# Optimization experiments

Measured on AMD Instinct MI355X. Metric: run time of the kernel, lower is better.

Reference implementation:

```python
import jax, jax.numpy as jnp
import numpy as np

N_NODES = 100000
N_EDGES = 1600000
IN_DIM, HID, OUT_DIM = 128, 64, 1


def _sage_conv(x, src, dst, wl, wr, b, num_nodes):
    # PyG SAGEConv (aggr='mean', root_weight=True):
    #   out = lin_l(mean_{j in N(i)} x_j) + lin_r(x_i), bias lives in lin_l
    msgs = x[src]                                                  # [E, d] gather
    agg = jax.ops.segment_sum(msgs, dst, num_segments=num_nodes)  # [N, d]
    deg = jax.ops.segment_sum(jnp.ones((src.shape[0],), x.dtype), dst,
                              num_segments=num_nodes)              # [N]
    agg = agg / jnp.maximum(deg, 1.0)[:, None]                     # mean aggregation
    return agg @ wl + x @ wr + b


def setup_inputs() -> dict:
    key = jax.random.key(0)
    ks = jax.random.split(key, 12)
    x = jax.random.normal(ks[0], (N_NODES, IN_DIM), dtype=jnp.float32)
    edge_index = jax.random.randint(ks[1], (2, N_EDGES), 0, N_NODES, dtype=jnp.int64)

    def glorot(k, fan_in, fan_out):
        s = jnp.sqrt(2.0 / (fan_in + fan_out)).astype(jnp.float32)
        return jax.random.normal(k, (fan_in, fan_out), dtype=jnp.float32) * s

    return {
        "x": x,
        "edge_index": edge_index,
        "wl0": glorot(ks[2], IN_DIM, HID), "wr0": glorot(ks[3], IN_DIM, HID),
        "b0": jnp.zeros((HID,), jnp.float32),
        "wl1": glorot(ks[4], HID, HID), "wr1": glorot(ks[5], HID, HID),
        "b1": jnp.zeros((HID,), jnp.float32),
        "wl2": glorot(ks[6], HID, OUT_DIM), "wr2": glorot(ks[7], HID, OUT_DIM),
        "b2": jnp.zeros((OUT_DIM,), jnp.float32),
    }


def reference(x, edge_index, wl0, wr0, b0, wl1, wr1, b1, wl2, wr2, b2):
    src, dst = edge_index[0], edge_index[1]
    n = x.shape[0]
    # layer 0: conv -> relu (dropout is identity in eval mode)
    h = jax.nn.relu(_sage_conv(x, src, dst, wl0, wr0, b0, n))
    # layer 1
    h = jax.nn.relu(_sage_conv(h, src, dst, wl1, wr1, b1, n))
    # final layer + sigmoid
    h = _sage_conv(h, src, dst, wl2, wr2, b2, n)
    return jax.nn.sigmoid(h)
```

## Files before the change

kernel.cpp:

```cpp
#include <hip/hip_runtime.h>
#include <hip/hip_bf16.h>
#include <math.h>


#define SHIFT 7
#define BKT 128
#define CHUNK 4096

typedef __bf16 bf16_t;
typedef bf16_t bf16x8 __attribute__((ext_vector_type(8)));
typedef float f32x4 __attribute__((ext_vector_type(4)));

__global__ __launch_bounds__(256) void zero_i(int* __restrict__ p, int n) {
    int i = blockIdx.x * 256 + threadIdx.x;
    if (i < n) p[i] = 0;
}

__global__ __launch_bounds__(256) void hist_bucket(const int* __restrict__ dstv,
                                                   int* __restrict__ bucket_cnt,
                                                   int E, int NB) {
    __shared__ int h[1024];
    for (int i = threadIdx.x; i < NB; i += 256) h[i] = 0;
    __syncthreads();
    int base = blockIdx.x * CHUNK;
#pragma unroll
    for (int k = 0; k < CHUNK / 256; ++k) {
        int e = base + threadIdx.x + k * 256;
        if (e < E) atomicAdd(&h[dstv[e] >> SHIFT], 1);
    }
    __syncthreads();
    for (int i = threadIdx.x; i < NB; i += 256)
        if (h[i]) atomicAdd(&bucket_cnt[i], h[i]);
}

__global__ __launch_bounds__(1024) void scan_bucket(const int* __restrict__ cnt,
                                                    int* __restrict__ boff,
                                                    int* __restrict__ bcur, int NB) {
    __shared__ int s[1024];
    int t = threadIdx.x;
    int v = (t < NB) ? cnt[t] : 0;
    s[t] = v;
    __syncthreads();
    for (int d = 1; d < 1024; d <<= 1) {
        int x = (t >= d) ? s[t - d] : 0;
        __syncthreads();
        s[t] += x;
        __syncthreads();
    }
    if (t < NB) {
        int o = s[t] - v;
        boff[t] = o;
        bcur[t] = o;
    }
    if (t == NB - 1) boff[NB] = s[t];
}

__global__ __launch_bounds__(256) void scatter_bucket(const int* __restrict__ srcv,
                                                      const int* __restrict__ dstv,
                                                      int* __restrict__ bcur,
                                                      int* __restrict__ bucketed,
                                                      int E, int NB) {
    __shared__ int hist[1024];
    __shared__ int offl[1024];
    __shared__ int basel[1024];
    __shared__ int partial[256];
    __shared__ int posA[CHUNK];
    __shared__ int valA[CHUNK];
    const int t = threadIdx.x;
    for (int i = t; i < NB; i += 256) hist[i] = 0;
    __syncthreads();

    const int cbase = blockIdx.x * CHUNK;
    int bk[CHUNK / 256], rk[CHUNK / 256], vv[CHUNK / 256];
#pragma unroll
    for (int k = 0; k < CHUNK / 256; ++k) {
        int e = cbase + t + k * 256;
        if (e < E) {
            int d = dstv[e];
            int s = srcv[e];
            int b = d >> SHIFT;
            bk[k] = b;
            rk[k] = atomicAdd(&hist[b], 1);
            vv[k] = (s << SHIFT) | (d & (BKT - 1));
        } else {
            bk[k] = -1;
        }
    }
    __syncthreads();

    for (int b = t; b < NB; b += 256) {
        int c = hist[b];
        basel[b] = c ? atomicAdd(&bcur[b], c) : 0;
    }
    {
        int g = t * 4;
        int a0 = (g + 0 < NB) ? hist[g + 0] : 0;
        int a1 = (g + 1 < NB) ? hist[g + 1] : 0;
        int a2 = (g + 2 < NB) ? hist[g + 2] : 0;
        int a3 = (g + 3 < NB) ? hist[g + 3] : 0;
        int sum = a0 + a1 + a2 + a3;
        partial[t] = sum;
        __syncthreads();
        for (int d = 1; d < 256; d <<= 1) {
            int x = (t >= d) ? partial[t - d] : 0;
            __syncthreads();
            partial[t] += x;
            __syncthreads();
        }
        int ex = partial[t] - sum;
        if (g + 0 < NB) offl[g + 0] = ex;
        if (g + 1 < NB) offl[g + 1] = ex + a0;
        if (g + 2 < NB) offl[g + 2] = ex + a0 + a1;
        if (g + 3 < NB) offl[g + 3] = ex + a0 + a1 + a2;
    }
    __syncthreads();

    int nloc = E - cbase;
    if (nloc > CHUNK) nloc = CHUNK;
#pragma unroll
    for (int k = 0; k < CHUNK / 256; ++k) {
        if (bk[k] >= 0) {
            int slot = offl[bk[k]] + rk[k];
            posA[slot] = basel[bk[k]] + rk[k];
            valA[slot] = vv[k];
        }
    }
    __syncthreads();
    for (int j = t; j < nloc; j += 256) bucketed[posA[j]] = valA[j];
}

__global__ __launch_bounds__(256) void sort_bucket(const int* __restrict__ bucketed,
                                                   const int* __restrict__ boff,
                                                   int* __restrict__ deg,
                                                   int* __restrict__ offs,
                                                   int* __restrict__ csr, int N) {
    __shared__ int cnt[BKT];
    __shared__ int sc[BKT];
    __shared__ int cur[BKT];
    const int b = blockIdx.x;
    const int t = threadIdx.x;
    const int ebase = boff[b], eend = boff[b + 1];
    if (t < BKT) cnt[t] = 0;
    __syncthreads();
    for (int i = ebase + t; i < eend; i += 256)
        atomicAdd(&cnt[bucketed[i] & (BKT - 1)], 1);
    __syncthreads();
    int v = (t < BKT) ? cnt[t] : 0;
    if (t < BKT) sc[t] = v;
    __syncthreads();
    for (int d = 1; d < BKT; d <<= 1) {
        int x = (t < BKT && t >= d) ? sc[t - d] : 0;
        __syncthreads();
        if (t < BKT) sc[t] += x;
        __syncthreads();
    }
    if (t < BKT) {
        int ex = sc[t] - v;
        cur[t] = ex;
        int dst = (b << SHIFT) + t;
        if (dst < N) {
            deg[dst] = v;
            offs[dst] = ebase + ex;
        }
    }
    __syncthreads();
    for (int i = ebase + t; i < eend; i += 256) {
        int w = bucketed[i];
        int p = atomicAdd(&cur[w & (BKT - 1)], 1);
        csr[ebase + p] = w >> SHIFT;
    }
}

__global__ __launch_bounds__(256) void prep_w(const float* __restrict__ wl0,
                                              const float* __restrict__ wr0,
                                              const float* __restrict__ wl1,
                                              const float* __restrict__ wr1,
                                              bf16_t* __restrict__ w0t,
                                              bf16_t* __restrict__ w1t) {
    int idx = blockIdx.x * 256 + threadIdx.x;
    if (idx < 128 * 128) {
        int j = idx >> 7, k = idx & 127;
        float v = (j < 64) ? wl0[k * 64 + j] : wr0[k * 64 + (j - 64)];
        w0t[idx] = (bf16_t)v;
    } else if (idx < 128 * 128 + 128 * 64) {
        int i2 = idx - 128 * 128;
        int j = i2 >> 6, k = i2 & 63;
        float v = (j < 64) ? wl1[k * 64 + j] : wr1[k * 64 + (j - 64)];
        w1t[i2] = (bf16_t)v;
    }
}

template <int KTOT, bool AIN_BF16>
__global__ __launch_bounds__(256) void gemm_mfma(const void* __restrict__ Ain,
                                                 const bf16_t* __restrict__ Wt,
                                                 bf16_t* __restrict__ Y, int N) {
    const int lane = threadIdx.x & 63;
    const int wv = threadIdx.x >> 6;
    const int r0 = blockIdx.x * 64 + wv * 16;
    const int rr = lane & 15;
    const int quad = lane >> 4;
    const int row_store = r0 + rr;
    int row = (row_store < N) ? row_store : (N - 1);
    constexpr int NK = KTOT / 32;

    bf16x8 xf[NK];
    if (AIN_BF16) {
        const bf16_t* A = (const bf16_t*)Ain;
#pragma unroll
        for (int kk = 0; kk < NK; ++kk)
            xf[kk] = *(const bf16x8*)&A[(size_t)row * KTOT + kk * 32 + quad * 8];
    } else {
        const float* A = (const float*)Ain;
#pragma unroll
        for (int kk = 0; kk < NK; ++kk) {
            const float* ap = &A[(size_t)row * KTOT + kk * 32 + quad * 8];
            float4 f0 = *(const float4*)ap;
            float4 f1 = *(const float4*)(ap + 4);
            union { bf16x8 v; bf16_t h[8]; } u;
            u.h[0] = (bf16_t)f0.x; u.h[1] = (bf16_t)f0.y;
            u.h[2] = (bf16_t)f0.z; u.h[3] = (bf16_t)f0.w;
            u.h[4] = (bf16_t)f1.x; u.h[5] = (bf16_t)f1.y;
            u.h[6] = (bf16_t)f1.z; u.h[7] = (bf16_t)f1.w;
            xf[kk] = u.v;
        }
    }

#pragma unroll
    for (int c = 0; c < 8; ++c) {
        f32x4 acc = {0.f, 0.f, 0.f, 0.f};
#pragma unroll
        for (int kk = 0; kk < NK; ++kk) {
            bf16x8 wf = *(const bf16x8*)&Wt[(size_t)(c * 16 + rr) * KTOT + kk * 32 + quad * 8];
            acc = __builtin_amdgcn_mfma_f32_16x16x32_bf16(wf, xf[kk], acc, 0, 0, 0);
        }
        if (row_store < N) {
            union { bf16_t h[4]; uint2 u; } p;
            p.h[0] = (bf16_t)acc[0]; p.h[1] = (bf16_t)acc[1];
            p.h[2] = (bf16_t)acc[2]; p.h[3] = (bf16_t)acc[3];
            *(uint2*)&Y[(size_t)row_store * 128 + c * 16 + quad * 4] = p.u;
        }
    }
}

template <bool FUSED>
__global__ __launch_bounds__(256) void agg_relu(const bf16_t* __restrict__ y,
                                                const int* __restrict__ csr,
                                                const int* __restrict__ offs,
                                                const int* __restrict__ deg,
                                                const float* __restrict__ bias,
                                                bf16_t* __restrict__ h,
                                                const float* __restrict__ wl2,
                                                const float* __restrict__ wr2,
                                                float* __restrict__ sl,
                                                float* __restrict__ sr, int N) {
    int wid = blockIdx.x * 4 + (threadIdx.x >> 6);
    if (wid >= N) return;
    const int lane = threadIdx.x & 63;
    const int half = lane >> 5;
    const int ch = (lane & 31) * 2;
    const int base = offs[wid];
    const int d = deg[wid];

    int sidx = (lane < d) ? csr[base + lane] : 0;

    int lastLane = (d > 0 && d - 1 < 64) ? (d - 1) : 0;
    int s_last = __shfl(sidx, lastLane);

    float ax = 0.f, ay = 0.f;
    const int npairs = d >> 1;
    const int pm = (npairs < 28) ? npairs : 28;
    int p = 0;
    for (; p + 4 <= pm; p += 4) {
        int s0 = __shfl(sidx, 2 * p + half);
        int s1 = __shfl(sidx, 2 * p + 2 + half);
        int s2 = __shfl(sidx, 2 * p + 4 + half);
        int s3 = __shfl(sidx, 2 * p + 6 + half);
        uint v0 = *(const uint*)&y[(size_t)s0 * 128 + ch];
        uint v1 = *(const uint*)&y[(size_t)s1 * 128 + ch];
        uint v2 = *(const uint*)&y[(size_t)s2 * 128 + ch];
        uint v3 = *(const uint*)&y[(size_t)s3 * 128 + ch];
        ax += __uint_as_float(v0 << 16) + __uint_as_float(v1 << 16) +
              __uint_as_float(v2 << 16) + __uint_as_float(v3 << 16);
        ay += __uint_as_float(v0 & 0xffff0000u) + __uint_as_float(v1 & 0xffff0000u) +
              __uint_as_float(v2 & 0xffff0000u) + __uint_as_float(v3 & 0xffff0000u);
    }
    for (; p < npairs; ++p) {
        int s0 = csr[base + 2 * p + half];
        uint v0 = *(const uint*)&y[(size_t)s0 * 128 + ch];
        ax += __uint_as_float(v0 << 16);
        ay += __uint_as_float(v0 & 0xffff0000u);
    }
    if ((d & 1) && half == 0) {
        int s0 = (d - 1 < 64) ? s_last : csr[base + d - 1];
        uint v0 = *(const uint*)&y[(size_t)s0 * 128 + ch];
        ax += __uint_as_float(v0 << 16);
        ay += __uint_as_float(v0 & 0xffff0000u);
    }
    ax += __shfl_xor(ax, 32);
    ay += __shfl_xor(ay, 32);

    float inv = 1.f / ((d > 0) ? (float)d : 1.f);
    uint vs = *(const uint*)&y[(size_t)wid * 128 + 64 + ch];
    float2 bv = *(const float2*)&bias[ch];
    float vx = fmaxf(ax * inv + __uint_as_float(vs << 16) + bv.x, 0.f);
    float vy = fmaxf(ay * inv + __uint_as_float(vs & 0xffff0000u) + bv.y, 0.f);

    if (!FUSED) {
        if (half == 0) {
            union { bf16_t b[2]; uint u; } pk;
            pk.b[0] = (bf16_t)vx;
            pk.b[1] = (bf16_t)vy;
            *(uint*)&h[(size_t)wid * 64 + ch] = pk.u;
        }
    } else {
        float a = vx * wl2[ch] + vy * wl2[ch + 1];
        float b = vx * wr2[ch] + vy * wr2[ch + 1];
#pragma unroll
        for (int off = 16; off; off >>= 1) {
            a += __shfl_xor(a, off);
            b += __shfl_xor(b, off);
        }
        if (lane == 0) {
            sl[wid] = a;
            sr[wid] = b;
        }
    }
}

__global__ __launch_bounds__(256) void final_k(const float* __restrict__ sl,
                                               const float* __restrict__ sr,
                                               const int* __restrict__ csr,
                                               const int* __restrict__ offs,
                                               const int* __restrict__ deg,
                                               const float* __restrict__ b2,
                                               float* __restrict__ out, int N) {
    int wid = blockIdx.x * 4 + (threadIdx.x >> 6);
    if (wid >= N) return;
    const int lane = threadIdx.x & 63;
    const int base = offs[wid];
    const int d = deg[wid];
    float acc = 0.f;
    for (int e = lane; e < d; e += 64) acc += sl[csr[base + e]];
#pragma unroll
    for (int off = 32; off; off >>= 1) acc += __shfl_xor(acc, off);
    if (lane == 0) {
        float m = (d > 0) ? (float)d : 1.f;
        float v = acc / m + sr[wid] + b2[0];
        out[wid] = 1.f / (1.f + expf(-v));
    }
}

extern "C" void kernel_launch(void* const* d_in, const int* in_sizes, int n_in,
                              void* d_out, int out_size, void* d_ws, size_t ws_size,
                              hipStream_t stream) {
    const float* x  = (const float*)d_in[0];
    const int*  ei  = (const int*)d_in[1];
    const float* wl0 = (const float*)d_in[2];
    const float* wr0 = (const float*)d_in[3];
    const float* b0  = (const float*)d_in[4];
    const float* wl1 = (const float*)d_in[5];
    const float* wr1 = (const float*)d_in[6];
    const float* b1  = (const float*)d_in[7];
    const float* wl2 = (const float*)d_in[8];
    const float* wr2 = (const float*)d_in[9];
    const float* b2  = (const float*)d_in[10];
    float* out = (float*)d_out;

    const int E = in_sizes[1] / 2;
    const int N = out_size;
    const int* srcv = ei;
    const int* dstv = ei + E;
    const int NB = (N + BKT - 1) >> SHIFT;

    char* ws = (char*)d_ws;
    size_t o = 0;
    auto take = [&](size_t nbytes) -> void* {
        void* p = ws + o;
        o = (o + nbytes + 255) & ~(size_t)255;
        return p;
    };
    int* deg    = (int*)take((size_t)N * 4);
    int* offs   = (int*)take((size_t)N * 4);
    int* bcnt   = (int*)take((size_t)(NB + 2) * 4);
    int* boff   = (int*)take((size_t)(NB + 2) * 4);
    int* bcur   = (int*)take((size_t)(NB + 2) * 4);
    int* csr    = (int*)take((size_t)E * 4);
    bf16_t* w0t = (bf16_t*)take(128 * 128 * 2);
    bf16_t* w1t = (bf16_t*)take(128 * 64 * 2);
    bf16_t* y   = (bf16_t*)take((size_t)N * 128 * 2);
    bf16_t* h   = (bf16_t*)take((size_t)N * 64 * 2);
    float* sl   = (float*)take((size_t)N * 4);
    float* sr   = (float*)take((size_t)N * 4);
    int* bucketed = (int*)y;
    (void)ws_size;

    const int nbC = (E + CHUNK - 1) / CHUNK;
    const int nbW = (N + 3) / 4;
    const int nbG = (N + 63) / 64;

    zero_i<<<(NB + 255) / 256, 256, 0, stream>>>(bcnt, NB);
    hist_bucket<<<nbC, 256, 0, stream>>>(dstv, bcnt, E, NB);
    scan_bucket<<<1, 1024, 0, stream>>>(bcnt, boff, bcur, NB);
    scatter_bucket<<<nbC, 256, 0, stream>>>(srcv, dstv, bcur, bucketed, E, NB);
    sort_bucket<<<NB, 256, 0, stream>>>(bucketed, boff, deg, offs, csr, N);

    prep_w<<<(128 * 128 + 128 * 64 + 255) / 256, 256, 0, stream>>>(wl0, wr0, wl1, wr1, w0t, w1t);

    gemm_mfma<128, false><<<nbG, 256, 0, stream>>>((const void*)x, w0t, y, N);
    agg_relu<false><<<nbW, 256, 0, stream>>>(y, csr, offs, deg, b0, h,
                                             nullptr, nullptr, nullptr, nullptr, N);
    gemm_mfma<64, true><<<nbG, 256, 0, stream>>>((const void*)h, w1t, y, N);
    agg_relu<true><<<nbW, 256, 0, stream>>>(y, csr, offs, deg, b1, nullptr,
                                            wl2, wr2, sl, sr, N);
    final_k<<<nbW, 256, 0, stream>>>(sl, sr, csr, offs, deg, b2, out, N);
}
```

Measured before the change: 330.4 us.

## Fold weight prep into histogram, pack offsets/degrees, widen gather unroll

Merges the weight-transpose kernel into the histogram launch as extra blocks, and replaces the zeroing kernel with a memset, removing two launches. Offsets and degrees are packed into a single int2 array so each aggregation wave does one load instead of two. The aggregation gather loop now issues 8 independent loads per iteration, with a single-step tail loop, and the cap on register-cached neighbor pairs rises from 28 to 32. This adds more in-flight loads per wave at the cost of extra registers.

```diff
diff --git a/kernel.cpp b/kernel.cpp
--- a/kernel.cpp
+++ b/kernel.cpp
@@ -11,14 +11,29 @@
 typedef bf16_t bf16x8 __attribute__((ext_vector_type(8)));
 typedef float f32x4 __attribute__((ext_vector_type(4)));
 
-__global__ __launch_bounds__(256) void zero_i(int* __restrict__ p, int n) {
-    int i = blockIdx.x * 256 + threadIdx.x;
-    if (i < n) p[i] = 0;
-}
-
 __global__ __launch_bounds__(256) void hist_bucket(const int* __restrict__ dstv,
                                                    int* __restrict__ bucket_cnt,
-                                                   int E, int NB) {
+                                                   int E, int NB, int nbC,
+                                                   const float* __restrict__ wl0,
+                                                   const float* __restrict__ wr0,
+                                                   const float* __restrict__ wl1,
+                                                   const float* __restrict__ wr1,
+                                                   bf16_t* __restrict__ w0t,
+                                                   bf16_t* __restrict__ w1t) {
+    if ((int)blockIdx.x >= nbC) {
+        int idx = (blockIdx.x - nbC) * 256 + threadIdx.x;
+        if (idx < 128 * 128) {
+            int j = idx >> 7, k = idx & 127;
+            float v = (j < 64) ? wl0[k * 64 + j] : wr0[k * 64 + (j - 64)];
+            w0t[idx] = (bf16_t)v;
+        } else if (idx < 128 * 128 + 128 * 64) {
+            int i2 = idx - 128 * 128;
+            int j = i2 >> 6, k = i2 & 63;
+            float v = (j < 64) ? wl1[k * 64 + j] : wr1[k * 64 + (j - 64)];
+            w1t[i2] = (bf16_t)v;
+        }
+        return;
+    }
     __shared__ int h[1024];
     for (int i = threadIdx.x; i < NB; i += 256) h[i] = 0;
     __syncthreads();
@@ -131,8 +146,7 @@
 
 __global__ __launch_bounds__(256) void sort_bucket(const int* __restrict__ bucketed,
                                                    const int* __restrict__ boff,
-                                                   int* __restrict__ deg,
-                                                   int* __restrict__ offs,
+                                                   int2* __restrict__ od,
                                                    int* __restrict__ csr, int N) {
     __shared__ int cnt[BKT];
     __shared__ int sc[BKT];
@@ -158,35 +172,13 @@
         int ex = sc[t] - v;
         cur[t] = ex;
         int dst = (b << SHIFT) + t;
-        if (dst < N) {
-            deg[dst] = v;
-            offs[dst] = ebase + ex;
-        }
+        if (dst < N) od[dst] = make_int2(ebase + ex, v);
     }
     __syncthreads();
     for (int i = ebase + t; i < eend; i += 256) {
         int w = bucketed[i];
         int p = atomicAdd(&cur[w & (BKT - 1)], 1);
         csr[ebase + p] = w >> SHIFT;
-    }
-}
-
-__global__ __launch_bounds__(256) void prep_w(const float* __restrict__ wl0,
-                                              const float* __restrict__ wr0,
-                                              const float* __restrict__ wl1,
-                                              const float* __restrict__ wr1,
-                                              bf16_t* __restrict__ w0t,
-                                              bf16_t* __restrict__ w1t) {
-    int idx = blockIdx.x * 256 + threadIdx.x;
-    if (idx < 128 * 128) {
-        int j = idx >> 7, k = idx & 127;
-        float v = (j < 64) ? wl0[k * 64 + j] : wr0[k * 64 + (j - 64)];
-        w0t[idx] = (bf16_t)v;
-    } else if (idx < 128 * 128 + 128 * 64) {
-        int i2 = idx - 128 * 128;
-        int j = i2 >> 6, k = i2 & 63;
-        float v = (j < 64) ? wl1[k * 64 + j] : wr1[k * 64 + (j - 64)];
-        w1t[i2] = (bf16_t)v;
     }
 }
 
@@ -245,8 +237,7 @@
 template <bool FUSED>
 __global__ __launch_bounds__(256) void agg_relu(const bf16_t* __restrict__ y,
                                                 const int* __restrict__ csr,
-                                                const int* __restrict__ offs,
-                                                const int* __restrict__ deg,
+                                                const int2* __restrict__ od,
                                                 const float* __restrict__ bias,
                                                 bf16_t* __restrict__ h,
                                                 const float* __restrict__ wl2,
@@ -258,8 +249,9 @@
     const int lane = threadIdx.x & 63;
     const int half = lane >> 5;
     const int ch = (lane & 31) * 2;
-    const int base = offs[wid];
-    const int d = deg[wid];
+    const int2 odv = od[wid];
+    const int base = odv.x;
+    const int d = odv.y;
 
     int sidx = (lane < d) ? csr[base + lane] : 0;
 
@@ -268,21 +260,26 @@
 
     float ax = 0.f, ay = 0.f;
     const int npairs = d >> 1;
-    const int pm = (npairs < 28) ? npairs : 28;
+    const int pm = (npairs < 32) ? npairs : 32;
     int p = 0;
-    for (; p + 4 <= pm; p += 4) {
+    for (; p + 8 <= pm; p += 8) {
+        int s[8];
+#pragma unroll
+        for (int j = 0; j < 8; ++j) s[j] = __shfl(sidx, 2 * (p + j) + half);
+        uint v[8];
+#pragma unroll
+        for (int j = 0; j < 8; ++j) v[j] = *(const uint*)&y[(size_t)s[j] * 128 + ch];
+#pragma unroll
+        for (int j = 0; j < 8; ++j) {
+            ax += __uint_as_float(v[j] << 16);
+            ay += __uint_as_float(v[j] & 0xffff0000u);
+        }
+    }
+    for (; p < pm; ++p) {
         int s0 = __shfl(sidx, 2 * p + half);
-        int s1 = __shfl(sidx, 2 * p + 2 + half);
-        int s2 = __shfl(sidx, 2 * p + 4 + half);
-        int s3 = __shfl(sidx, 2 * p + 6 + half);
         uint v0 = *(const uint*)&y[(size_t)s0 * 128 + ch];
-        uint v1 = *(const uint*)&y[(size_t)s1 * 128 + ch];
-        uint v2 = *(const uint*)&y[(size_t)s2 * 128 + ch];
-        uint v3 = *(const uint*)&y[(size_t)s3 * 128 + ch];
-        ax += __uint_as_float(v0 << 16) + __uint_as_float(v1 << 16) +
-              __uint_as_float(v2 << 16) + __uint_as_float(v3 << 16);
-        ay += __uint_as_float(v0 & 0xffff0000u) + __uint_as_float(v1 & 0xffff0000u) +
-              __uint_as_float(v2 & 0xffff0000u) + __uint_as_float(v3 & 0xffff0000u);
+        ax += __uint_as_float(v0 << 16);
+        ay += __uint_as_float(v0 & 0xffff0000u);
     }
     for (; p < npairs; ++p) {
         int s0 = csr[base + 2 * p + half];
@@ -330,15 +327,15 @@
 __global__ __launch_bounds__(256) void final_k(const float* __restrict__ sl,
                                                const float* __restrict__ sr,
                                                const int* __restrict__ csr,
-                                               const int* __restrict__ offs,
-                                               const int* __restrict__ deg,
+                                               const int2* __restrict__ od,
                                                const float* __restrict__ b2,
                                                float* __restrict__ out, int N) {
     int wid = blockIdx.x * 4 + (threadIdx.x >> 6);
     if (wid >= N) return;
     const int lane = threadIdx.x & 63;
-    const int base = offs[wid];
-    const int d = deg[wid];
+    const int2 odv = od[wid];
+    const int base = odv.x;
+    const int d = odv.y;
     float acc = 0.f;
     for (int e = lane; e < d; e += 64) acc += sl[csr[base + e]];
 #pragma unroll
@@ -379,8 +376,7 @@
         o = (o + nbytes + 255) & ~(size_t)255;
         return p;
     };
-    int* deg    = (int*)take((size_t)N * 4);
-    int* offs   = (int*)take((size_t)N * 4);
+    int2* od    = (int2*)take((size_t)N * 8);
     int* bcnt   = (int*)take((size_t)(NB + 2) * 4);
     int* boff   = (int*)take((size_t)(NB + 2) * 4);
     int* bcur   = (int*)take((size_t)(NB + 2) * 4);
@@ -395,22 +391,22 @@
     (void)ws_size;
 
     const int nbC = (E + CHUNK - 1) / CHUNK;
+    const int nbP = (128 * 128 + 128 * 64 + 255) / 256;
     const int nbW = (N + 3) / 4;
     const int nbG = (N + 63) / 64;
 
-    zero_i<<<(NB + 255) / 256, 256, 0, stream>>>(bcnt, NB);
-    hist_bucket<<<nbC, 256, 0, stream>>>(dstv, bcnt, E, NB);
+    hipMemsetAsync(bcnt, 0, (size_t)NB * 4, stream);
+    hist_bucket<<<nbC + nbP, 256, 0, stream>>>(dstv, bcnt, E, NB, nbC,
+                                               wl0, wr0, wl1, wr1, w0t, w1t);
     scan_bucket<<<1, 1024, 0, stream>>>(bcnt, boff, bcur, NB);
     scatter_bucket<<<nbC, 256, 0, stream>>>(srcv, dstv, bcur, bucketed, E, NB);
-    sort_bucket<<<NB, 256, 0, stream>>>(bucketed, boff, deg, offs, csr, N);
-
-    prep_w<<<(128 * 128 + 128 * 64 + 255) / 256, 256, 0, stream>>>(wl0, wr0, wl1, wr1, w0t, w1t);
+    sort_bucket<<<NB, 256, 0, stream>>>(bucketed, boff, od, csr, N);
 
     gemm_mfma<128, false><<<nbG, 256, 0, stream>>>((const void*)x, w0t, y, N);
-    agg_relu<false><<<nbW, 256, 0, stream>>>(y, csr, offs, deg, b0, h,
+    agg_relu<false><<<nbW, 256, 0, stream>>>(y, csr, od, b0, h,
                                              nullptr, nullptr, nullptr, nullptr, N);
     gemm_mfma<64, true><<<nbG, 256, 0, stream>>>((const void*)h, w1t, y, N);
-    agg_relu<true><<<nbW, 256, 0, stream>>>(y, csr, offs, deg, b1, nullptr,
+    agg_relu<true><<<nbW, 256, 0, stream>>>(y, csr, od, b1, nullptr,
                                             wl2, wr2, sl, sr, N);
-    final_k<<<nbW, 256, 0, stream>>>(sl, sr, csr, offs, deg, b2, out, N);
-}
+    final_k<<<nbW, 256, 0, stream>>>(sl, sr, csr, od, b2, out, N);
+}
```

After: 330.7 us. No clear change (+0.1%).
